# Performance work log

Hardware: AMD Instinct MI355X
Metric: run time of the kernel (lower is better)

## Reference

```python
import jax, jax.numpy as jnp
import numpy as np

N1, E1 = 102400, 300000
N2, E2 = 10240, 40960
N3, E3 = 1024, 4096
G = 64
D = 256   # node_dim == hidden_dim (forced by where(M==0, x, M))
B = 64    # bond_dim
DEPTHS = (3, 3, 4)


def _make_edges(rng, n_nodes, n_edges):
    # build mirrored directed edges so every edge has an exact reverse
    half = n_edges // 2
    u = rng.integers(0, n_nodes, half)
    v = rng.integers(0, n_nodes, half)
    src = np.concatenate([u, v])
    dst = np.concatenate([v, u])
    rev = np.concatenate([np.arange(half, n_edges), np.arange(0, half)])
    return np.stack([src, dst]).astype(np.int64), rev.astype(np.int64)


def _linear_params(key, fan_in, fan_out):
    k1, k2 = jax.random.split(key)
    s = 1.0 / np.sqrt(fan_in)
    W = jax.random.uniform(k1, (fan_in, fan_out), jnp.float32, -s, s)
    b = jax.random.uniform(k2, (fan_out,), jnp.float32, -s, s)
    return W, b


def setup_inputs() -> dict:
    rng = np.random.default_rng(0)
    key = jax.random.key(0)
    ks = jax.random.split(key, 16)

    ei1, rev1 = _make_edges(rng, N1, E1)
    ei2, rev2 = _make_edges(rng, N2, E2)
    ei3, rev3 = _make_edges(rng, N3, E3)

    inp = {
        "x": jax.random.normal(ks[0], (N1, D), jnp.float32),
        "edge_attr1": jax.random.normal(ks[1], (E1, B), jnp.float32),
        "edge_attr2": jax.random.normal(ks[2], (E2, B), jnp.float32),
        "edge_attr3": jax.random.normal(ks[3], (E3, B), jnp.float32),
        "edge_index1": jnp.asarray(ei1), "rev_edge_index1": jnp.asarray(rev1),
        "edge_index2": jnp.asarray(ei2), "rev_edge_index2": jnp.asarray(rev2),
        "edge_index3": jnp.asarray(ei3), "rev_edge_index3": jnp.asarray(rev3),
        "batch1_2": jnp.asarray(np.repeat(np.arange(N2), N1 // N2)),
        "batch2": jnp.asarray(np.repeat(np.arange(N3), N2 // N3)),
        "batch3": jnp.asarray(np.repeat(np.arange(G), N3 // G)),
    }
    kidx = 4
    for lvl in (1, 2, 3):
        Wi, bi = _linear_params(ks[kidx], D + B, D); kidx += 1
        Wh, bh = _linear_params(ks[kidx], D, D); kidx += 1
        Wo, bo = _linear_params(ks[kidx], D + D, D); kidx += 1
        inp[f"Wi{lvl}"], inp[f"bi{lvl}"] = Wi, bi
        inp[f"Wh{lvl}"], inp[f"bh{lvl}"] = Wh, bh
        inp[f"Wo{lvl}"], inp[f"bo{lvl}"] = Wo, bo
    return inp


def _bmp(x, src, dst, rev, ea, Wi, bi, Wh, bh, Wo, bo, depth):
    # BondMessagePassing.forward (dropout is identity in eval)
    n = x.shape[0]
    H0 = jax.nn.relu(jnp.concatenate([x[src], ea], axis=1) @ Wi + bi)  # [E, D]
    H = H0
    for _ in range(depth - 1):
        agg = jax.ops.segment_sum(H, dst, num_segments=n)              # [N, D]
        M = agg[src] - H[rev]
        H = jax.nn.relu(H0 + M @ Wh + bh)
    M = jax.ops.segment_sum(H, dst, num_segments=n)
    M = jnp.where(jnp.sum(M, axis=1, keepdims=True) == 0, x, M)
    return jax.nn.relu(jnp.concatenate([x, M], axis=1) @ Wo + bo)


def _mean_pool(h, seg, n):
    s = jax.ops.segment_sum(h, seg, num_segments=n)
    c = jax.ops.segment_sum(jnp.ones((h.shape[0], 1), h.dtype), seg, num_segments=n)
    return s / jnp.maximum(c, 1.0)


def reference(x, edge_attr1, edge_attr2, edge_attr3,
              edge_index1, rev_edge_index1, edge_index2, rev_edge_index2,
              edge_index3, rev_edge_index3, batch1_2, batch2, batch3,
              Wi1, bi1, Wh1, bh1, Wo1, bo1,
              Wi2, bi2, Wh2, bh2, Wo2, bo2,
              Wi3, bi3, Wh3, bh3, Wo3, bo3):
    h1 = _bmp(x, edge_index1[0], edge_index1[1], rev_edge_index1, edge_attr1,
              Wi1, bi1, Wh1, bh1, Wo1, bo1, DEPTHS[0])
    x2 = _mean_pool(h1, batch1_2, N2)
    h2 = _bmp(x2, edge_index2[0], edge_index2[1], rev_edge_index2, edge_attr2,
              Wi2, bi2, Wh2, bh2, Wo2, bo2, DEPTHS[1])
    x3 = _mean_pool(h2, batch2, N3)
    h3 = _bmp(x3, edge_index3[0], edge_index3[1], rev_edge_index3, edge_attr3,
              Wi3, bi3, Wh3, bh3, Wo3, bo3, DEPTHS[2])
    out = _mean_pool(h3, batch3, G)  # [G, D] subgraph3_pooled
    return out
```

## Files before the change

### kernel.cpp

```cpp
#include <hip/hip_runtime.h>
#include <stdint.h>

typedef __bf16 bf16;
typedef __bf16 bf16x4 __attribute__((ext_vector_type(4)));
typedef __bf16 bf16x8 __attribute__((ext_vector_type(8)));
typedef float  f32x4  __attribute__((ext_vector_type(4)));

__device__ __forceinline__ int clampi(int v, int n) { return (v < 0 || v >= n) ? 0 : v; }

__global__ void wtcvt_kernel(const float* __restrict__ W, bf16* __restrict__ Wt, int K) {
  int idx = blockIdx.x * 256 + threadIdx.x;
  if (idx >= K * 256) return;
  int k = idx >> 8, n = idx & 255;
  Wt[(size_t)n * K + k] = (bf16)W[idx];
}

__global__ void hist_kernel(const int* __restrict__ dst, int E, int* __restrict__ cnt, int N) {
  int e = blockIdx.x * 256 + threadIdx.x;
  if (e < E) atomicAdd(&cnt[clampi(dst[e], N)], 1);
}

__global__ void scan_block_kernel(const int* __restrict__ cnt, int N,
                                  int* __restrict__ incl, int* __restrict__ bsums) {
  __shared__ int sd[256];
  int t = threadIdx.x, bid = blockIdx.x;
  int base = bid * 1024 + t * 4;
  int v0 = (base + 0 < N) ? cnt[base + 0] : 0;
  int v1 = (base + 1 < N) ? cnt[base + 1] : 0;
  int v2 = (base + 2 < N) ? cnt[base + 2] : 0;
  int v3 = (base + 3 < N) ? cnt[base + 3] : 0;
  int s1 = v0 + v1, s2 = s1 + v2, s3 = s2 + v3;
  sd[t] = s3;
  __syncthreads();
  for (int off = 1; off < 256; off <<= 1) {
    int x = 0;
    if (t >= off) x = sd[t - off];
    __syncthreads();
    sd[t] += x;
    __syncthreads();
  }
  int excl = sd[t] - s3;
  if (base + 0 < N) incl[base + 0] = excl + v0;
  if (base + 1 < N) incl[base + 1] = excl + s1;
  if (base + 2 < N) incl[base + 2] = excl + s2;
  if (base + 3 < N) incl[base + 3] = excl + s3;
  if (t == 255) bsums[bid] = sd[255];
}

__global__ void scan_sums_kernel(const int* __restrict__ bsums, int nb, int* __restrict__ bexcl) {
  __shared__ int sd[256];
  int t = threadIdx.x;
  int v = (t < nb) ? bsums[t] : 0;
  sd[t] = v;
  __syncthreads();
  for (int off = 1; off < 256; off <<= 1) {
    int x = 0;
    if (t >= off) x = sd[t - off];
    __syncthreads();
    sd[t] += x;
    __syncthreads();
  }
  if (t < nb) bexcl[t] = sd[t] - v;
}

__global__ void scan_add_kernel(const int* __restrict__ incl, const int* __restrict__ bexcl,
                                int N, int* __restrict__ offs) {
  int i = blockIdx.x * 256 + threadIdx.x;
  if (i < N) offs[i + 1] = incl[i] + bexcl[i >> 10];
  if (i == 0) offs[0] = 0;
}

__global__ void scatter_kernel(const int* __restrict__ dst, int E, const int* __restrict__ offs,
                               int* __restrict__ cursor, int* __restrict__ elist, int N) {
  int e = blockIdx.x * 256 + threadIdx.x;
  if (e < E) {
    int d = clampi(dst[e], N);
    int p = atomicAdd(&cursor[d], 1);
    elist[offs[d] + p] = e;
  }
}

template <int WHERE, int XF32>
__global__ void segsum_kernel(const bf16* __restrict__ H, const int* __restrict__ elist,
                              const int* __restrict__ offs, const float* __restrict__ xf,
                              const bf16* __restrict__ xb, bf16* __restrict__ out, int N) {
  int lane = threadIdx.x & 63;
  int node = blockIdx.x * 4 + (threadIdx.x >> 6);
  if (node >= N) return;
  int beg = offs[node], end = offs[node + 1];
  float a0 = 0.f, a1 = 0.f, a2 = 0.f, a3 = 0.f;
  for (int p = beg; p < end; ++p) {
    int e = elist[p];
    bf16x4 v = ((const bf16x4*)(H + (size_t)e * 256))[lane];
    a0 += (float)v[0]; a1 += (float)v[1]; a2 += (float)v[2]; a3 += (float)v[3];
  }
  if (WHERE) {
    float s = a0 + a1 + a2 + a3;
    for (int off = 1; off < 64; off <<= 1) s += __shfl_xor(s, off);
    if (s == 0.f) {
      bf16x4 o;
      if (XF32) {
        float4 xv = ((const float4*)(xf))[(size_t)node * 64 + lane];
        o[0] = (bf16)xv.x; o[1] = (bf16)xv.y; o[2] = (bf16)xv.z; o[3] = (bf16)xv.w;
      } else {
        o = ((const bf16x4*)(xb + (size_t)node * 256))[lane];
      }
      ((bf16x4*)(out + (size_t)node * 256))[lane] = o;
      return;
    }
  }
  bf16x4 o = {(bf16)a0, (bf16)a1, (bf16)a2, (bf16)a3};
  ((bf16x4*)(out + (size_t)node * 256))[lane] = o;
}

template <int OUTF32>
__global__ void pool_kernel(const bf16* __restrict__ h, bf16* __restrict__ outb,
                            float* __restrict__ outf, int Nout, int cnt) {
  int lane = threadIdx.x & 63;
  int node = blockIdx.x * 4 + (threadIdx.x >> 6);
  if (node >= Nout) return;
  float a0 = 0.f, a1 = 0.f, a2 = 0.f, a3 = 0.f;
  size_t base = (size_t)node * cnt;
  for (int p = 0; p < cnt; ++p) {
    bf16x4 v = ((const bf16x4*)(h + (base + p) * 256))[lane];
    a0 += (float)v[0]; a1 += (float)v[1]; a2 += (float)v[2]; a3 += (float)v[3];
  }
  float c = (float)cnt;
  a0 /= c; a1 /= c; a2 /= c; a3 /= c;
  if (OUTF32) {
    float4 o = {a0, a1, a2, a3};
    ((float4*)(outf + (size_t)node * 256))[lane] = o;
  } else {
    bf16x4 o = {(bf16)a0, (bf16)a1, (bf16)a2, (bf16)a3};
    ((bf16x4*)(outb + (size_t)node * 256))[lane] = o;
  }
}

template <int MODE, int XF32>
__global__ __launch_bounds__(256, 2) void gemm_kernel(
    const float* __restrict__ A1f, const bf16* __restrict__ A1b,
    const float* __restrict__ A2f, const bf16* __restrict__ A2b,
    const bf16* __restrict__ Wt, const float* __restrict__ bias, const bf16* H0,
    const int* __restrict__ srcIdx, const int* __restrict__ revIdx,
    bf16* out, int Mrows, int K, int Nsrc) {
  __shared__ __align__(16) bf16 As[128 * 64];
  __shared__ __align__(16) bf16 Bs[128 * 64];
  int tid = threadIdx.x;
  int lane = tid & 63;
  int wave = tid >> 6;
  int wm = wave >> 1, wn = wave & 1;
  int m0 = blockIdx.x * 128;
  int n0 = blockIdx.y * 128;

  f32x4 acc[4][4];
#pragma unroll
  for (int i = 0; i < 4; ++i)
#pragma unroll
    for (int j = 0; j < 4; ++j) acc[i][j] = (f32x4){0.f, 0.f, 0.f, 0.f};

  int nk = K / 64;
  for (int kc = 0; kc < nk; ++kc) {
    int k0 = kc * 64;
    __syncthreads();
#pragma unroll
    for (int r = 0; r < 4; ++r) {
      int unit = r * 256 + tid;
      int row = unit >> 3, u = unit & 7, us = u ^ (row & 7);
      bf16x8 v = *(const bf16x8*)(Wt + (size_t)(n0 + row) * K + k0 + u * 8);
      *(bf16x8*)(&Bs[(size_t)(row * 8 + us) * 8]) = v;
    }
#pragma unroll
    for (int r = 0; r < 4; ++r) {
      int unit = r * 256 + tid;
      int row = unit >> 3, u = unit & 7, us = u ^ (row & 7);
      int rr = m0 + row;
      if (rr >= Mrows) rr = Mrows - 1;
      bf16x8 v;
      if (MODE == 0) {
        if (k0 < 256) {
          int sn = clampi(srcIdx[rr], Nsrc);
          if (XF32) {
            const float* g = A1f + (size_t)sn * 256 + k0 + u * 8;
            float4 a = *(const float4*)g, b = *(const float4*)(g + 4);
            v[0] = (bf16)a.x; v[1] = (bf16)a.y; v[2] = (bf16)a.z; v[3] = (bf16)a.w;
            v[4] = (bf16)b.x; v[5] = (bf16)b.y; v[6] = (bf16)b.z; v[7] = (bf16)b.w;
          } else {
            v = *(const bf16x8*)(A1b + (size_t)sn * 256 + k0 + u * 8);
          }
        } else {
          const float* g = A2f + (size_t)rr * 64 + (k0 - 256) + u * 8;
          float4 a = *(const float4*)g, b = *(const float4*)(g + 4);
          v[0] = (bf16)a.x; v[1] = (bf16)a.y; v[2] = (bf16)a.z; v[3] = (bf16)a.w;
          v[4] = (bf16)b.x; v[5] = (bf16)b.y; v[6] = (bf16)b.z; v[7] = (bf16)b.w;
        }
      } else if (MODE == 1) {
        int sn = clampi(srcIdx[rr], Nsrc);
        int rv = clampi(revIdx[rr], Mrows);
        bf16x8 va = *(const bf16x8*)(A1b + (size_t)sn * 256 + k0 + u * 8);
        bf16x8 vh = *(const bf16x8*)(A2b + (size_t)rv * 256 + k0 + u * 8);
#pragma unroll
        for (int j = 0; j < 8; ++j) v[j] = (bf16)((float)va[j] - (float)vh[j]);
      } else {
        if (k0 < 256) {
          if (XF32) {
            const float* g = A1f + (size_t)rr * 256 + k0 + u * 8;
            float4 a = *(const float4*)g, b = *(const float4*)(g + 4);
            v[0] = (bf16)a.x; v[1] = (bf16)a.y; v[2] = (bf16)a.z; v[3] = (bf16)a.w;
            v[4] = (bf16)b.x; v[5] = (bf16)b.y; v[6] = (bf16)b.z; v[7] = (bf16)b.w;
          } else {
            v = *(const bf16x8*)(A1b + (size_t)rr * 256 + k0 + u * 8);
          }
        } else {
          v = *(const bf16x8*)(A2b + (size_t)rr * 256 + (k0 - 256) + u * 8);
        }
      }
      *(bf16x8*)(&As[(size_t)(row * 8 + us) * 8]) = v;
    }
    __syncthreads();
#pragma unroll
    for (int s = 0; s < 2; ++s) {
      int kq = s * 4 + (lane >> 4);
      bf16x8 af[4], bfr[4];
#pragma unroll
      for (int i = 0; i < 4; ++i) {
        int arow = wm * 64 + i * 16 + (lane & 15);
        af[i] = *(const bf16x8*)(&As[(size_t)arow * 64 + (size_t)(kq ^ (arow & 7)) * 8]);
      }
#pragma unroll
      for (int j = 0; j < 4; ++j) {
        int brow = wn * 64 + j * 16 + (lane & 15);
        bfr[j] = *(const bf16x8*)(&Bs[(size_t)brow * 64 + (size_t)(kq ^ (brow & 7)) * 8]);
      }
#pragma unroll
      for (int i = 0; i < 4; ++i)
#pragma unroll
        for (int j = 0; j < 4; ++j)
          acc[i][j] = __builtin_amdgcn_mfma_f32_16x16x32_bf16(af[i], bfr[j], acc[i][j], 0, 0, 0);
    }
  }
#pragma unroll
  for (int i = 0; i < 4; ++i) {
    int rbase = m0 + wm * 64 + i * 16 + ((lane >> 4) << 2);
#pragma unroll
    for (int j = 0; j < 4; ++j) {
      int col = n0 + wn * 64 + j * 16 + (lane & 15);
      float bcol = bias[col];
#pragma unroll
      for (int r = 0; r < 4; ++r) {
        int row = rbase + r;
        if (row < Mrows) {
          float v = acc[i][j][r] + bcol;
          if (MODE == 1) v += (float)H0[(size_t)row * 256 + col];
          v = fmaxf(v, 0.f);
          out[(size_t)row * 256 + col] = (bf16)v;
        }
      }
    }
  }
}

template <int XF32>
static void run_level(const float* xf, const bf16* xb, const float* ea,
                      const int* src, const int* dst, const int* rev, int E, int N, int depth,
                      const bf16* WiT, const float* bi_, const bf16* WhT, const float* bh_,
                      const bf16* WoT, const float* bo_,
                      bf16* C, bf16* Dd, bf16* Ee, bf16* agg, bf16* h,
                      int* cnt, int* incl, int* offs, int* cursr, int* bsums, int* bexcl,
                      int* elist, hipStream_t stream) {
  hipMemsetAsync(cnt, 0, (size_t)N * 4, stream);
  hist_kernel<<<(E + 255) / 256, 256, 0, stream>>>(dst, E, cnt, N);
  int nb = (N + 1023) / 1024;
  scan_block_kernel<<<nb, 256, 0, stream>>>(cnt, N, incl, bsums);
  scan_sums_kernel<<<1, 256, 0, stream>>>(bsums, nb, bexcl);
  scan_add_kernel<<<(N + 255) / 256, 256, 0, stream>>>(incl, bexcl, N, offs);
  hipMemsetAsync(cursr, 0, (size_t)N * 4, stream);
  scatter_kernel<<<(E + 255) / 256, 256, 0, stream>>>(dst, E, offs, cursr, elist, N);

  dim3 ge((E + 127) / 128, 2);
  gemm_kernel<0, XF32><<<ge, 256, 0, stream>>>(xf, xb, ea, nullptr, WiT, bi_, nullptr, src,
                                               nullptr, C, E, 320, N);
  bf16* Hcur = C;
  for (int it = 0; it < depth - 1; ++it) {
    segsum_kernel<0, 0><<<(N + 3) / 4, 256, 0, stream>>>(Hcur, elist, offs, nullptr, nullptr,
                                                         agg, N);
    bf16* Hn = (it == depth - 2) ? C : ((it & 1) ? Ee : Dd);
    gemm_kernel<1, 0><<<ge, 256, 0, stream>>>(nullptr, agg, nullptr, Hcur, WhT, bh_, C, src,
                                              rev, Hn, E, 256, N);
    Hcur = Hn;
  }
  segsum_kernel<1, XF32><<<(N + 3) / 4, 256, 0, stream>>>(Hcur, elist, offs, xf, xb, agg, N);
  dim3 gn((N + 127) / 128, 2);
  gemm_kernel<2, XF32><<<gn, 256, 0, stream>>>(xf, xb, nullptr, agg, WoT, bo_, nullptr, nullptr,
                                               nullptr, h, N, 512, N);
}

extern "C" void kernel_launch(void* const* d_in, const int* in_sizes, int n_in,
                              void* d_out, int out_size, void* d_ws, size_t ws_size,
                              hipStream_t stream) {
  constexpr int N1 = 102400, E1 = 300000;
  constexpr int N2 = 10240, E2 = 40960;
  constexpr int N3 = 1024, E3 = 4096;
  constexpr int G = 64;
  constexpr int KI = 320, KH = 256, KO = 512;

  const float* x   = (const float*)d_in[0];
  const float* ea1 = (const float*)d_in[1];
  const float* ea2 = (const float*)d_in[2];
  const float* ea3 = (const float*)d_in[3];
  const int* ei1 = (const int*)d_in[4];
  const int* rv1 = (const int*)d_in[5];
  const int* ei2 = (const int*)d_in[6];
  const int* rv2 = (const int*)d_in[7];
  const int* ei3 = (const int*)d_in[8];
  const int* rv3 = (const int*)d_in[9];
  const float *Wi[3], *bi[3], *Wh[3], *bh[3], *Wo[3], *bo[3];
  for (int l = 0; l < 3; ++l) {
    Wi[l] = (const float*)d_in[13 + 6 * l + 0];
    bi[l] = (const float*)d_in[13 + 6 * l + 1];
    Wh[l] = (const float*)d_in[13 + 6 * l + 2];
    bh[l] = (const float*)d_in[13 + 6 * l + 3];
    Wo[l] = (const float*)d_in[13 + 6 * l + 4];
    bo[l] = (const float*)d_in[13 + 6 * l + 5];
  }
  float* outp = (float*)d_out;
  char* ws = (char*)d_ws;

  size_t off = 0;
  auto alloc = [&](size_t b) { size_t o = off; off += (b + 255) & ~(size_t)255; return o; };
  size_t o_wit[3], o_wht[3], o_wot[3];
  for (int l = 0; l < 3; ++l) {
    o_wit[l] = alloc((size_t)256 * KI * 2);
    o_wht[l] = alloc((size_t)256 * KH * 2);
    o_wot[l] = alloc((size_t)256 * KO * 2);
  }
  size_t o_C   = alloc((size_t)E1 * 256 * 2);
  size_t o_D   = alloc((size_t)E1 * 256 * 2);
  size_t o_E3b = alloc((size_t)E3 * 256 * 2);
  size_t o_agg = alloc((size_t)N1 * 256 * 2);
  size_t o_x2  = alloc((size_t)N2 * 256 * 2);
  size_t o_h2  = alloc((size_t)N2 * 256 * 2);
  size_t o_x3  = alloc((size_t)N3 * 256 * 2);
  size_t o_h3  = alloc((size_t)N3 * 256 * 2);
  size_t o_cnt = alloc((size_t)N1 * 4);
  size_t o_inc = alloc((size_t)N1 * 4);
  size_t o_off = alloc((size_t)(N1 + 1) * 4);
  size_t o_cur = alloc((size_t)N1 * 4);
  size_t o_bs  = alloc(1024 * 4);
  size_t o_bx  = alloc(1024 * 4);
  size_t o_el  = alloc((size_t)E1 * 4);

  if (ws_size < off) {
    hipMemsetAsync(d_out, 0, (size_t)out_size * 4, stream);
    return;
  }

  int* cnt   = (int*)(ws + o_cnt);
  int* incl  = (int*)(ws + o_inc);
  int* offs  = (int*)(ws + o_off);
  int* cursr = (int*)(ws + o_cur);
  int* bsums = (int*)(ws + o_bs);
  int* bexcl = (int*)(ws + o_bx);
  int* elist = (int*)(ws + o_el);
  bf16* C    = (bf16*)(ws + o_C);
  bf16* Dd   = (bf16*)(ws + o_D);
  bf16* E3b  = (bf16*)(ws + o_E3b);
  bf16* agg  = (bf16*)(ws + o_agg);
  bf16* x2b  = (bf16*)(ws + o_x2);
  bf16* h2b  = (bf16*)(ws + o_h2);
  bf16* x3b  = (bf16*)(ws + o_x3);
  bf16* h3b  = (bf16*)(ws + o_h3);

  for (int l = 0; l < 3; ++l) {
    wtcvt_kernel<<<(KI * 256 + 255) / 256, 256, 0, stream>>>(Wi[l], (bf16*)(ws + o_wit[l]), KI);
    wtcvt_kernel<<<(KH * 256 + 255) / 256, 256, 0, stream>>>(Wh[l], (bf16*)(ws + o_wht[l]), KH);
    wtcvt_kernel<<<(KO * 256 + 255) / 256, 256, 0, stream>>>(Wo[l], (bf16*)(ws + o_wot[l]), KO);
  }

  run_level<1>(x, nullptr, ea1, ei1, ei1 + E1, rv1, E1, N1, 3,
               (bf16*)(ws + o_wit[0]), bi[0], (bf16*)(ws + o_wht[0]), bh[0],
               (bf16*)(ws + o_wot[0]), bo[0], C, Dd, Dd, agg, C,
               cnt, incl, offs, cursr, bsums, bexcl, elist, stream);
  pool_kernel<0><<<(N2 + 3) / 4, 256, 0, stream>>>(C, x2b, nullptr, N2, N1 / N2);

  run_level<0>(nullptr, x2b, ea2, ei2, ei2 + E2, rv2, E2, N2, 3,
               (bf16*)(ws + o_wit[1]), bi[1], (bf16*)(ws + o_wht[1]), bh[1],
               (bf16*)(ws + o_wot[1]), bo[1], C, Dd, Dd, agg, h2b,
               cnt, incl, offs, cursr, bsums, bexcl, elist, stream);
  pool_kernel<0><<<(N3 + 3) / 4, 256, 0, stream>>>(h2b, x3b, nullptr, N3, N2 / N3);

  run_level<0>(nullptr, x3b, ea3, ei3, ei3 + E3, rv3, E3, N3, 4,
               (bf16*)(ws + o_wit[2]), bi[2], (bf16*)(ws + o_wht[2]), bh[2],
               (bf16*)(ws + o_wot[2]), bo[2], C, Dd, E3b, agg, h3b,
               cnt, incl, offs, cursr, bsums, bexcl, elist, stream);
  pool_kernel<1><<<(G + 3) / 4, 256, 0, stream>>>(h3b, nullptr, outp, G, N3 / G);
}
```

Before: 1.436 ms.

## Widen GEMM tile to full output width with async B loads and A prefetch

The GEMM now uses 512-thread blocks covering all 256 output columns, so each gathered A row is fetched once instead of twice across two column blocks. B tiles are loaded directly into LDS with global_load_lds, and the next K-chunk's A data is prefetched into registers while MFMAs run on the current chunk. Gather indices are computed once per block. The costs are more LDS per block (As plus a doubled Bs), more register pressure from the prefetch buffers, and a harder occupancy target of 4 blocks of 512 threads.

```diff
diff --git a/kernel.cpp b/kernel.cpp
--- a/kernel.cpp
+++ b/kernel.cpp
@@ -7,6 +7,11 @@
 typedef float  f32x4  __attribute__((ext_vector_type(4)));
 
 __device__ __forceinline__ int clampi(int v, int n) { return (v < 0 || v >= n) ? 0 : v; }
+
+__device__ __forceinline__ void gload16(const void* g, void* l) {
+  __builtin_amdgcn_global_load_lds((const __attribute__((address_space(1))) void*)g,
+                                   (__attribute__((address_space(3))) void*)l, 16, 0, 0);
+}
 
 __global__ void wtcvt_kernel(const float* __restrict__ W, bf16* __restrict__ Wt, int K) {
   int idx = blockIdx.x * 256 + threadIdx.x;
@@ -137,20 +142,40 @@
 }
 
 template <int MODE, int XF32>
-__global__ __launch_bounds__(256, 2) void gemm_kernel(
+__global__ __launch_bounds__(512, 4) void gemm_kernel(
     const float* __restrict__ A1f, const bf16* __restrict__ A1b,
     const float* __restrict__ A2f, const bf16* __restrict__ A2b,
     const bf16* __restrict__ Wt, const float* __restrict__ bias, const bf16* H0,
     const int* __restrict__ srcIdx, const int* __restrict__ revIdx,
     bf16* out, int Mrows, int K, int Nsrc) {
   __shared__ __align__(16) bf16 As[128 * 64];
-  __shared__ __align__(16) bf16 Bs[128 * 64];
+  __shared__ __align__(16) bf16 Bs[256 * 64];
   int tid = threadIdx.x;
   int lane = tid & 63;
   int wave = tid >> 6;
-  int wm = wave >> 1, wn = wave & 1;
+  int wm = wave >> 2, wn = wave & 3;
   int m0 = blockIdx.x * 128;
-  int n0 = blockIdx.y * 128;
+
+  int rowA[2], uA[2];
+  int base1[2], base2[2];
+#pragma unroll
+  for (int r = 0; r < 2; ++r) {
+    int unit = r * 512 + tid;
+    rowA[r] = unit >> 3;
+    uA[r] = unit & 7;
+    int rr = m0 + rowA[r];
+    if (rr >= Mrows) rr = Mrows - 1;
+    if (MODE == 0) {
+      base1[r] = clampi(srcIdx[rr], Nsrc) * 256;
+      base2[r] = rr * 64;
+    } else if (MODE == 1) {
+      base1[r] = clampi(srcIdx[rr], Nsrc) * 256;
+      base2[r] = clampi(revIdx[rr], Mrows) * 256;
+    } else {
+      base1[r] = rr * 256;
+      base2[r] = rr * 256;
+    }
+  }
 
   f32x4 acc[4][4];
 #pragma unroll
@@ -158,65 +183,92 @@
 #pragma unroll
     for (int j = 0; j < 4; ++j) acc[i][j] = (f32x4){0.f, 0.f, 0.f, 0.f};
 
-  int nk = K / 64;
-  for (int kc = 0; kc < nk; ++kc) {
+  float4 pf[2][2];
+
+  auto loadA = [&](int kc) {
     int k0 = kc * 64;
-    __syncthreads();
-#pragma unroll
-    for (int r = 0; r < 4; ++r) {
-      int unit = r * 256 + tid;
-      int row = unit >> 3, u = unit & 7, us = u ^ (row & 7);
-      bf16x8 v = *(const bf16x8*)(Wt + (size_t)(n0 + row) * K + k0 + u * 8);
-      *(bf16x8*)(&Bs[(size_t)(row * 8 + us) * 8]) = v;
-    }
-#pragma unroll
-    for (int r = 0; r < 4; ++r) {
-      int unit = r * 256 + tid;
-      int row = unit >> 3, u = unit & 7, us = u ^ (row & 7);
-      int rr = m0 + row;
-      if (rr >= Mrows) rr = Mrows - 1;
-      bf16x8 v;
+#pragma unroll
+    for (int r = 0; r < 2; ++r) {
+      int u8 = uA[r] * 8;
       if (MODE == 0) {
         if (k0 < 256) {
-          int sn = clampi(srcIdx[rr], Nsrc);
           if (XF32) {
-            const float* g = A1f + (size_t)sn * 256 + k0 + u * 8;
-            float4 a = *(const float4*)g, b = *(const float4*)(g + 4);
-            v[0] = (bf16)a.x; v[1] = (bf16)a.y; v[2] = (bf16)a.z; v[3] = (bf16)a.w;
-            v[4] = (bf16)b.x; v[5] = (bf16)b.y; v[6] = (bf16)b.z; v[7] = (bf16)b.w;
+            const float* g = A1f + (size_t)(base1[r] + k0 + u8);
+            pf[r][0] = *(const float4*)g;
+            pf[r][1] = *(const float4*)(g + 4);
           } else {
-            v = *(const bf16x8*)(A1b + (size_t)sn * 256 + k0 + u * 8);
+            pf[r][0] = *(const float4*)(A1b + (size_t)(base1[r] + k0 + u8));
           }
         } else {
-          const float* g = A2f + (size_t)rr * 64 + (k0 - 256) + u * 8;
-          float4 a = *(const float4*)g, b = *(const float4*)(g + 4);
-          v[0] = (bf16)a.x; v[1] = (bf16)a.y; v[2] = (bf16)a.z; v[3] = (bf16)a.w;
-          v[4] = (bf16)b.x; v[5] = (bf16)b.y; v[6] = (bf16)b.z; v[7] = (bf16)b.w;
+          const float* g = A2f + (size_t)(base2[r] + u8);
+          pf[r][0] = *(const float4*)g;
+          pf[r][1] = *(const float4*)(g + 4);
         }
       } else if (MODE == 1) {
-        int sn = clampi(srcIdx[rr], Nsrc);
-        int rv = clampi(revIdx[rr], Mrows);
-        bf16x8 va = *(const bf16x8*)(A1b + (size_t)sn * 256 + k0 + u * 8);
-        bf16x8 vh = *(const bf16x8*)(A2b + (size_t)rv * 256 + k0 + u * 8);
-#pragma unroll
-        for (int j = 0; j < 8; ++j) v[j] = (bf16)((float)va[j] - (float)vh[j]);
+        pf[r][0] = *(const float4*)(A1b + (size_t)(base1[r] + k0 + u8));
+        pf[r][1] = *(const float4*)(A2b + (size_t)(base2[r] + k0 + u8));
       } else {
         if (k0 < 256) {
           if (XF32) {
-            const float* g = A1f + (size_t)rr * 256 + k0 + u * 8;
-            float4 a = *(const float4*)g, b = *(const float4*)(g + 4);
-            v[0] = (bf16)a.x; v[1] = (bf16)a.y; v[2] = (bf16)a.z; v[3] = (bf16)a.w;
-            v[4] = (bf16)b.x; v[5] = (bf16)b.y; v[6] = (bf16)b.z; v[7] = (bf16)b.w;
+            const float* g = A1f + (size_t)(base1[r] + k0 + u8);
+            pf[r][0] = *(const float4*)g;
+            pf[r][1] = *(const float4*)(g + 4);
           } else {
-            v = *(const bf16x8*)(A1b + (size_t)rr * 256 + k0 + u * 8);
+            pf[r][0] = *(const float4*)(A1b + (size_t)(base1[r] + k0 + u8));
           }
         } else {
-          v = *(const bf16x8*)(A2b + (size_t)rr * 256 + (k0 - 256) + u * 8);
+          pf[r][0] = *(const float4*)(A2b + (size_t)(base2[r] + (k0 - 256) + u8));
         }
       }
+    }
+  };
+
+  auto writeA = [&](int kc) {
+    int k0 = kc * 64;
+#pragma unroll
+    for (int r = 0; r < 2; ++r) {
+      int row = rowA[r], us = uA[r] ^ (row & 7);
+      bf16x8 v;
+      bool cvt32;
+      if (MODE == 0) cvt32 = XF32 || (k0 >= 256);
+      else if (MODE == 2) cvt32 = XF32 && (k0 < 256);
+      else cvt32 = false;
+      if (MODE == 1) {
+        bf16x8 va = *(bf16x8*)(&pf[r][0]);
+        bf16x8 vh = *(bf16x8*)(&pf[r][1]);
+#pragma unroll
+        for (int j = 0; j < 8; ++j) v[j] = (bf16)((float)va[j] - (float)vh[j]);
+      } else if (cvt32) {
+        const float* f = (const float*)&pf[r][0];
+#pragma unroll
+        for (int j = 0; j < 8; ++j) v[j] = (bf16)f[j];
+      } else {
+        v = *(bf16x8*)(&pf[r][0]);
+      }
       *(bf16x8*)(&As[(size_t)(row * 8 + us) * 8]) = v;
     }
-    __syncthreads();
+  };
+
+  auto loadB = [&](int kc) {
+    int k0 = kc * 64;
+#pragma unroll
+    for (int r = 0; r < 4; ++r) {
+      int unit = r * 512 + tid;
+      int row = unit >> 3, us = (unit & 7) ^ (row & 7);
+      const bf16* g = Wt + (size_t)row * K + k0 + us * 8;
+      bf16* l = &Bs[(size_t)(r * 512 + wave * 64) * 8];
+      gload16(g, l);
+    }
+  };
+
+  int nk = K / 64;
+  loadA(0);
+  for (int kc = 0; kc < nk; ++kc) {
+    __syncthreads();
+    writeA(kc);
+    loadB(kc);
+    __syncthreads();
+    if (kc + 1 < nk) loadA(kc + 1);
 #pragma unroll
     for (int s = 0; s < 2; ++s) {
       int kq = s * 4 + (lane >> 4);
@@ -243,7 +295,7 @@
     int rbase = m0 + wm * 64 + i * 16 + ((lane >> 4) << 2);
 #pragma unroll
     for (int j = 0; j < 4; ++j) {
-      int col = n0 + wn * 64 + j * 16 + (lane & 15);
+      int col = wn * 64 + j * 16 + (lane & 15);
       float bcol = bias[col];
 #pragma unroll
       for (int r = 0; r < 4; ++r) {
@@ -276,21 +328,21 @@
   hipMemsetAsync(cursr, 0, (size_t)N * 4, stream);
   scatter_kernel<<<(E + 255) / 256, 256, 0, stream>>>(dst, E, offs, cursr, elist, N);
 
-  dim3 ge((E + 127) / 128, 2);
-  gemm_kernel<0, XF32><<<ge, 256, 0, stream>>>(xf, xb, ea, nullptr, WiT, bi_, nullptr, src,
+  dim3 ge((E + 127) / 128);
+  gemm_kernel<0, XF32><<<ge, 512, 0, stream>>>(xf, xb, ea, nullptr, WiT, bi_, nullptr, src,
                                                nullptr, C, E, 320, N);
   bf16* Hcur = C;
   for (int it = 0; it < depth - 1; ++it) {
     segsum_kernel<0, 0><<<(N + 3) / 4, 256, 0, stream>>>(Hcur, elist, offs, nullptr, nullptr,
                                                          agg, N);
     bf16* Hn = (it == depth - 2) ? C : ((it & 1) ? Ee : Dd);
-    gemm_kernel<1, 0><<<ge, 256, 0, stream>>>(nullptr, agg, nullptr, Hcur, WhT, bh_, C, src,
+    gemm_kernel<1, 0><<<ge, 512, 0, stream>>>(nullptr, agg, nullptr, Hcur, WhT, bh_, C, src,
                                               rev, Hn, E, 256, N);
     Hcur = Hn;
   }
   segsum_kernel<1, XF32><<<(N + 3) / 4, 256, 0, stream>>>(Hcur, elist, offs, xf, xb, agg, N);
-  dim3 gn((N + 127) / 128, 2);
-  gemm_kernel<2, XF32><<<gn, 256, 0, stream>>>(xf, xb, nullptr, agg, WoT, bo_, nullptr, nullptr,
+  dim3 gn((N + 127) / 128);
+  gemm_kernel<2, XF32><<<gn, 512, 0, stream>>>(xf, xb, nullptr, agg, WoT, bo_, nullptr, nullptr,
                                                nullptr, h, N, 512, N);
 }
 
```

Result: faster. 1.290 ms (-10.2%).

## Restructure GEMMs to load full-K A tile once and split concatenated weights

Applied to the files above, without the earlier changes.

Replaces the single templated GEMM, which used a 2D grid over column halves and a K loop, with a full-row kernel. Each block now loads its whole 128x256 A tile (the gathered, or gathered-minus-reverse, rows) into LDS once and reuses it for both 128-column halves of the output, so the irregular gather is no longer repeated per column block. Weight tiles are fetched with direct global-to-LDS loads. The concatenated-input GEMMs are split into two passes, an edge-attribute GEMM and an x GEMM, with the first result added in the second pass's epilogue. This adds an extra round trip of a bf16 intermediate through global memory and uses about 128KB of LDS per block, which limits occupancy.

```diff
diff --git a/kernel.cpp b/kernel.cpp
--- a/kernel.cpp
+++ b/kernel.cpp
@@ -8,11 +8,17 @@
 
 __device__ __forceinline__ int clampi(int v, int n) { return (v < 0 || v >= n) ? 0 : v; }
 
-__global__ void wtcvt_kernel(const float* __restrict__ W, bf16* __restrict__ Wt, int K) {
+__device__ __forceinline__ void gload16(const void* g, void* l) {
+  __builtin_amdgcn_global_load_lds((const __attribute__((address_space(1))) void*)g,
+                                   (__attribute__((address_space(3))) void*)l, 16, 0, 0);
+}
+
+__global__ void wtcvtT_kernel(const float* __restrict__ W, bf16* __restrict__ Wt,
+                              int krows, int krow0) {
   int idx = blockIdx.x * 256 + threadIdx.x;
-  if (idx >= K * 256) return;
+  if (idx >= krows * 256) return;
   int k = idx >> 8, n = idx & 255;
-  Wt[(size_t)n * K + k] = (bf16)W[idx];
+  Wt[(size_t)n * krows + k] = (bf16)W[(size_t)(krow0 + k) * 256 + n];
 }
 
 __global__ void hist_kernel(const int* __restrict__ dst, int E, int* __restrict__ cnt, int N) {
@@ -136,134 +142,217 @@
   }
 }
 
-template <int MODE, int XF32>
-__global__ __launch_bounds__(256, 2) void gemm_kernel(
-    const float* __restrict__ A1f, const bf16* __restrict__ A1b,
-    const float* __restrict__ A2f, const bf16* __restrict__ A2b,
-    const bf16* __restrict__ Wt, const float* __restrict__ bias, const bf16* H0,
-    const int* __restrict__ srcIdx, const int* __restrict__ revIdx,
-    bf16* out, int Mrows, int K, int Nsrc) {
+__global__ __launch_bounds__(512) void gemm_ea(
+    const float* __restrict__ ea, const bf16* __restrict__ Wt ,
+    const float* __restrict__ bias, bf16* __restrict__ out, int Mrows) {
   __shared__ __align__(16) bf16 As[128 * 64];
-  __shared__ __align__(16) bf16 Bs[128 * 64];
-  int tid = threadIdx.x;
-  int lane = tid & 63;
-  int wave = tid >> 6;
-  int wm = wave >> 1, wn = wave & 1;
-  int m0 = blockIdx.x * 128;
-  int n0 = blockIdx.y * 128;
-
+  __shared__ __align__(16) bf16 Bs[256 * 64];
+  const int tid = threadIdx.x;
+  const int lane = tid & 63;
+  const int wave = tid >> 6;
+  const int wm = wave >> 2, wn = wave & 3;
+  const int m0 = blockIdx.x * 128;
+
+#pragma unroll
+  for (int r = 0; r < 2; ++r) {
+    int unit = r * 512 + tid;
+    int row = unit >> 3, u = unit & 7;
+    int rr = m0 + row;
+    if (rr >= Mrows) rr = Mrows - 1;
+    const float* g = ea + (size_t)rr * 64 + u * 8;
+    float4 a = *(const float4*)g, b = *(const float4*)(g + 4);
+    bf16x8 v = {(bf16)a.x, (bf16)a.y, (bf16)a.z, (bf16)a.w,
+                (bf16)b.x, (bf16)b.y, (bf16)b.z, (bf16)b.w};
+    int pos = u ^ (row & 7);
+    *(bf16x8*)(&As[((size_t)row * 8 + pos) * 8]) = v;
+  }
+#pragma unroll
+  for (int r = 0; r < 4; ++r) {
+    int unit = r * 512 + tid;
+    int col = unit >> 3, u = unit & 7;
+    int us = u ^ (col & 7);
+    gload16(Wt + (size_t)col * 64 + us * 8, &Bs[(size_t)(r * 512 + wave * 64) * 8]);
+  }
   f32x4 acc[4][4];
 #pragma unroll
   for (int i = 0; i < 4; ++i)
 #pragma unroll
     for (int j = 0; j < 4; ++j) acc[i][j] = (f32x4){0.f, 0.f, 0.f, 0.f};
-
-  int nk = K / 64;
-  for (int kc = 0; kc < nk; ++kc) {
-    int k0 = kc * 64;
-    __syncthreads();
-#pragma unroll
-    for (int r = 0; r < 4; ++r) {
-      int unit = r * 256 + tid;
-      int row = unit >> 3, u = unit & 7, us = u ^ (row & 7);
-      bf16x8 v = *(const bf16x8*)(Wt + (size_t)(n0 + row) * K + k0 + u * 8);
-      *(bf16x8*)(&Bs[(size_t)(row * 8 + us) * 8]) = v;
-    }
-#pragma unroll
-    for (int r = 0; r < 4; ++r) {
-      int unit = r * 256 + tid;
-      int row = unit >> 3, u = unit & 7, us = u ^ (row & 7);
-      int rr = m0 + row;
-      if (rr >= Mrows) rr = Mrows - 1;
-      bf16x8 v;
-      if (MODE == 0) {
-        if (k0 < 256) {
-          int sn = clampi(srcIdx[rr], Nsrc);
-          if (XF32) {
-            const float* g = A1f + (size_t)sn * 256 + k0 + u * 8;
-            float4 a = *(const float4*)g, b = *(const float4*)(g + 4);
-            v[0] = (bf16)a.x; v[1] = (bf16)a.y; v[2] = (bf16)a.z; v[3] = (bf16)a.w;
-            v[4] = (bf16)b.x; v[5] = (bf16)b.y; v[6] = (bf16)b.z; v[7] = (bf16)b.w;
-          } else {
-            v = *(const bf16x8*)(A1b + (size_t)sn * 256 + k0 + u * 8);
-          }
-        } else {
-          const float* g = A2f + (size_t)rr * 64 + (k0 - 256) + u * 8;
-          float4 a = *(const float4*)g, b = *(const float4*)(g + 4);
-          v[0] = (bf16)a.x; v[1] = (bf16)a.y; v[2] = (bf16)a.z; v[3] = (bf16)a.w;
-          v[4] = (bf16)b.x; v[5] = (bf16)b.y; v[6] = (bf16)b.z; v[7] = (bf16)b.w;
-        }
-      } else if (MODE == 1) {
-        int sn = clampi(srcIdx[rr], Nsrc);
-        int rv = clampi(revIdx[rr], Mrows);
-        bf16x8 va = *(const bf16x8*)(A1b + (size_t)sn * 256 + k0 + u * 8);
-        bf16x8 vh = *(const bf16x8*)(A2b + (size_t)rv * 256 + k0 + u * 8);
-#pragma unroll
-        for (int j = 0; j < 8; ++j) v[j] = (bf16)((float)va[j] - (float)vh[j]);
-      } else {
-        if (k0 < 256) {
-          if (XF32) {
-            const float* g = A1f + (size_t)rr * 256 + k0 + u * 8;
-            float4 a = *(const float4*)g, b = *(const float4*)(g + 4);
-            v[0] = (bf16)a.x; v[1] = (bf16)a.y; v[2] = (bf16)a.z; v[3] = (bf16)a.w;
-            v[4] = (bf16)b.x; v[5] = (bf16)b.y; v[6] = (bf16)b.z; v[7] = (bf16)b.w;
-          } else {
-            v = *(const bf16x8*)(A1b + (size_t)rr * 256 + k0 + u * 8);
-          }
-        } else {
-          v = *(const bf16x8*)(A2b + (size_t)rr * 256 + (k0 - 256) + u * 8);
-        }
-      }
-      *(bf16x8*)(&As[(size_t)(row * 8 + us) * 8]) = v;
-    }
-    __syncthreads();
-#pragma unroll
-    for (int s = 0; s < 2; ++s) {
-      int kq = s * 4 + (lane >> 4);
-      bf16x8 af[4], bfr[4];
-#pragma unroll
-      for (int i = 0; i < 4; ++i) {
-        int arow = wm * 64 + i * 16 + (lane & 15);
-        af[i] = *(const bf16x8*)(&As[(size_t)arow * 64 + (size_t)(kq ^ (arow & 7)) * 8]);
-      }
-#pragma unroll
-      for (int j = 0; j < 4; ++j) {
-        int brow = wn * 64 + j * 16 + (lane & 15);
-        bfr[j] = *(const bf16x8*)(&Bs[(size_t)brow * 64 + (size_t)(kq ^ (brow & 7)) * 8]);
-      }
-#pragma unroll
-      for (int i = 0; i < 4; ++i)
-#pragma unroll
-        for (int j = 0; j < 4; ++j)
-          acc[i][j] = __builtin_amdgcn_mfma_f32_16x16x32_bf16(af[i], bfr[j], acc[i][j], 0, 0, 0);
-    }
+  __syncthreads();
+#pragma unroll
+  for (int s = 0; s < 2; ++s) {
+    int kq = s * 4 + (lane >> 4);
+    bf16x8 af[4], bfr[4];
+#pragma unroll
+    for (int i = 0; i < 4; ++i) {
+      int ar = wm * 64 + i * 16 + (lane & 15);
+      af[i] = *(const bf16x8*)(&As[((size_t)ar * 8 + (kq ^ (ar & 7))) * 8]);
+    }
+#pragma unroll
+    for (int j = 0; j < 4; ++j) {
+      int bc = wn * 64 + j * 16 + (lane & 15);
+      bfr[j] = *(const bf16x8*)(&Bs[((size_t)bc * 8 + (kq ^ (bc & 7))) * 8]);
+    }
+#pragma unroll
+    for (int i = 0; i < 4; ++i)
+#pragma unroll
+      for (int j = 0; j < 4; ++j)
+        acc[i][j] = __builtin_amdgcn_mfma_f32_16x16x32_bf16(af[i], bfr[j], acc[i][j], 0, 0, 0);
   }
 #pragma unroll
   for (int i = 0; i < 4; ++i) {
     int rbase = m0 + wm * 64 + i * 16 + ((lane >> 4) << 2);
 #pragma unroll
     for (int j = 0; j < 4; ++j) {
-      int col = n0 + wn * 64 + j * 16 + (lane & 15);
+      int col = wn * 64 + j * 16 + (lane & 15);
       float bcol = bias[col];
 #pragma unroll
       for (int r = 0; r < 4; ++r) {
         int row = rbase + r;
-        if (row < Mrows) {
-          float v = acc[i][j][r] + bcol;
-          if (MODE == 1) v += (float)H0[(size_t)row * 256 + col];
-          v = fmaxf(v, 0.f);
-          out[(size_t)row * 256 + col] = (bf16)v;
+        if (row < Mrows) out[(size_t)row * 256 + col] = (bf16)(acc[i][j][r] + bcol);
+      }
+    }
+  }
+}
+
+template <int SRC, int XF32, int ADDROW, int RELU>
+__global__ __launch_bounds__(512) void gemm_fullB(
+    const float* __restrict__ Af, const bf16* __restrict__ Ab, const bf16* __restrict__ Hb,
+    const bf16* __restrict__ Wt , const float* __restrict__ bias,
+    const bf16* __restrict__ addrow, const int* __restrict__ srcIdx,
+    const int* __restrict__ revIdx, bf16* out, int Mrows, int Nsrc) {
+  __shared__ __align__(16) bf16 As[128 * 256];
+  __shared__ __align__(16) bf16 Bs[128 * 256];
+  const int tid = threadIdx.x;
+  const int lane = tid & 63;
+  const int wave = tid >> 6;
+  const int wm = wave >> 2, wn = wave & 3;
+  const int m0 = blockIdx.x * 128;
+
+  const int rid = tid >> 3, lane8 = tid & 7;
+#pragma unroll
+  for (int rp = 0; rp < 2; ++rp) {
+    int row = rp * 64 + rid;
+    int rr = m0 + row;
+    if (rr >= Mrows) rr = Mrows - 1;
+    int swz = lane8 ^ (row & 7);
+    if (SRC == 2) {
+      const bf16* ga = Ab + (size_t)clampi(srcIdx[rr], Nsrc) * 256;
+      const bf16* gh = Hb + (size_t)clampi(revIdx[rr], Mrows) * 256;
+      float4 pa[4], ph[4];
+#pragma unroll
+      for (int st = 0; st < 4; ++st) {
+        pa[st] = *(const float4*)(ga + (lane8 + 8 * st) * 8);
+        ph[st] = *(const float4*)(gh + (lane8 + 8 * st) * 8);
+      }
+#pragma unroll
+      for (int st = 0; st < 4; ++st) {
+        bf16x8 va = *(bf16x8*)&pa[st];
+        bf16x8 vh = *(bf16x8*)&ph[st];
+        bf16x8 v;
+#pragma unroll
+        for (int j = 0; j < 8; ++j) v[j] = (bf16)((float)va[j] - (float)vh[j]);
+        *(bf16x8*)(&As[((size_t)row * 32 + st * 8 + swz) * 8]) = v;
+      }
+    } else {
+      int rsrc = (SRC == 1) ? clampi(srcIdx[rr], Nsrc) : rr;
+      if (XF32) {
+        const float* g = Af + (size_t)rsrc * 256;
+        float4 p[4][2];
+#pragma unroll
+        for (int st = 0; st < 4; ++st) {
+          const float* gg = g + (lane8 + 8 * st) * 8;
+          p[st][0] = *(const float4*)gg;
+          p[st][1] = *(const float4*)(gg + 4);
         }
-      }
-    }
+#pragma unroll
+        for (int st = 0; st < 4; ++st) {
+          const float* f = (const float*)&p[st][0];
+          bf16x8 v;
+#pragma unroll
+          for (int j = 0; j < 8; ++j) v[j] = (bf16)f[j];
+          *(bf16x8*)(&As[((size_t)row * 32 + st * 8 + swz) * 8]) = v;
+        }
+      } else {
+        const bf16* g = Ab + (size_t)rsrc * 256;
+        float4 p[4];
+#pragma unroll
+        for (int st = 0; st < 4; ++st) p[st] = *(const float4*)(g + (lane8 + 8 * st) * 8);
+#pragma unroll
+        for (int st = 0; st < 4; ++st)
+          *(bf16x8*)(&As[((size_t)row * 32 + st * 8 + swz) * 8]) = *(bf16x8*)&p[st];
+      }
+    }
+  }
+
+  f32x4 acc[4][2];
+#pragma unroll
+  for (int p = 0; p < 2; ++p) {
+#pragma unroll
+    for (int r = 0; r < 8; ++r) {
+      int unit = r * 512 + tid;
+      int col = unit >> 5, cu = unit & 31;
+      int cus = (cu & 24) | ((cu & 7) ^ (col & 7));
+      gload16(Wt + (size_t)(p * 128 + col) * 256 + cus * 8,
+              &Bs[(size_t)(r * 512 + wave * 64) * 8]);
+    }
+#pragma unroll
+    for (int i = 0; i < 4; ++i)
+#pragma unroll
+      for (int j = 0; j < 2; ++j) acc[i][j] = (f32x4){0.f, 0.f, 0.f, 0.f};
+    __syncthreads();
+#pragma unroll
+    for (int kc = 0; kc < 4; ++kc) {
+#pragma unroll
+      for (int s = 0; s < 2; ++s) {
+        int kq = s * 4 + (lane >> 4);
+        bf16x8 af[4], bfr[2];
+#pragma unroll
+        for (int i = 0; i < 4; ++i) {
+          int ar = wm * 64 + i * 16 + (lane & 15);
+          af[i] = *(const bf16x8*)(&As[((size_t)ar * 32 + kc * 8 + (kq ^ (ar & 7))) * 8]);
+        }
+#pragma unroll
+        for (int j = 0; j < 2; ++j) {
+          int bc = wn * 32 + j * 16 + (lane & 15);
+          bfr[j] = *(const bf16x8*)(&Bs[((size_t)bc * 32 + kc * 8 + (kq ^ (bc & 7))) * 8]);
+        }
+#pragma unroll
+        for (int i = 0; i < 4; ++i)
+#pragma unroll
+          for (int j = 0; j < 2; ++j)
+            acc[i][j] = __builtin_amdgcn_mfma_f32_16x16x32_bf16(af[i], bfr[j], acc[i][j], 0, 0, 0);
+      }
+    }
+#pragma unroll
+    for (int i = 0; i < 4; ++i) {
+      int rbase = m0 + wm * 64 + i * 16 + ((lane >> 4) << 2);
+#pragma unroll
+      for (int j = 0; j < 2; ++j) {
+        int col = p * 128 + wn * 32 + j * 16 + (lane & 15);
+        float bcol = bias ? bias[col] : 0.f;
+#pragma unroll
+        for (int r = 0; r < 4; ++r) {
+          int row = rbase + r;
+          if (row < Mrows) {
+            float v = acc[i][j][r] + bcol;
+            if (ADDROW) v += (float)addrow[(size_t)row * 256 + col];
+            if (RELU) v = fmaxf(v, 0.f);
+            out[(size_t)row * 256 + col] = (bf16)v;
+          }
+        }
+      }
+    }
+    if (p == 0) __syncthreads();
   }
 }
 
 template <int XF32>
 static void run_level(const float* xf, const bf16* xb, const float* ea,
                       const int* src, const int* dst, const int* rev, int E, int N, int depth,
-                      const bf16* WiT, const float* bi_, const bf16* WhT, const float* bh_,
-                      const bf16* WoT, const float* bo_,
+                      const bf16* WixT, const bf16* WieT, const float* bi_,
+                      const bf16* WhT, const float* bh_,
+                      const bf16* WoxT, const bf16* WomT, const float* bo_,
                       bf16* C, bf16* Dd, bf16* Ee, bf16* agg, bf16* h,
                       int* cnt, int* incl, int* offs, int* cursr, int* bsums, int* bexcl,
                       int* elist, hipStream_t stream) {
@@ -276,22 +365,25 @@
   hipMemsetAsync(cursr, 0, (size_t)N * 4, stream);
   scatter_kernel<<<(E + 255) / 256, 256, 0, stream>>>(dst, E, offs, cursr, elist, N);
 
-  dim3 ge((E + 127) / 128, 2);
-  gemm_kernel<0, XF32><<<ge, 256, 0, stream>>>(xf, xb, ea, nullptr, WiT, bi_, nullptr, src,
-                                               nullptr, C, E, 320, N);
+  dim3 ge((E + 127) / 128);
+  gemm_ea<<<ge, 512, 0, stream>>>(ea, WieT, bi_, Dd, E);
+  gemm_fullB<1, XF32, 1, 1><<<ge, 512, 0, stream>>>(xf, xb, nullptr, WixT, nullptr, Dd, src,
+                                                    nullptr, C, E, N);
   bf16* Hcur = C;
   for (int it = 0; it < depth - 1; ++it) {
     segsum_kernel<0, 0><<<(N + 3) / 4, 256, 0, stream>>>(Hcur, elist, offs, nullptr, nullptr,
                                                          agg, N);
     bf16* Hn = (it == depth - 2) ? C : ((it & 1) ? Ee : Dd);
-    gemm_kernel<1, 0><<<ge, 256, 0, stream>>>(nullptr, agg, nullptr, Hcur, WhT, bh_, C, src,
-                                              rev, Hn, E, 256, N);
+    gemm_fullB<2, 0, 1, 1><<<ge, 512, 0, stream>>>(nullptr, agg, Hcur, WhT, bh_, C, src, rev,
+                                                   Hn, E, N);
     Hcur = Hn;
   }
   segsum_kernel<1, XF32><<<(N + 3) / 4, 256, 0, stream>>>(Hcur, elist, offs, xf, xb, agg, N);
-  dim3 gn((N + 127) / 128, 2);
-  gemm_kernel<2, XF32><<<gn, 256, 0, stream>>>(xf, xb, nullptr, agg, WoT, bo_, nullptr, nullptr,
-                                               nullptr, h, N, 512, N);
+  dim3 gn((N + 127) / 128);
+  gemm_fullB<0, XF32, 0, 0><<<gn, 512, 0, stream>>>(xf, xb, nullptr, WoxT, bo_, nullptr,
+                                                    nullptr, nullptr, Dd, N, N);
+  gemm_fullB<0, 0, 1, 1><<<gn, 512, 0, stream>>>(nullptr, agg, nullptr, WomT, nullptr, Dd,
+                                                 nullptr, nullptr, h, N, N);
 }
 
 extern "C" void kernel_launch(void* const* d_in, const int* in_sizes, int n_in,
@@ -301,7 +393,6 @@
   constexpr int N2 = 10240, E2 = 40960;
   constexpr int N3 = 1024, E3 = 4096;
   constexpr int G = 64;
-  constexpr int KI = 320, KH = 256, KO = 512;
 
   const float* x   = (const float*)d_in[0];
   const float* ea1 = (const float*)d_in[1];
@@ -327,11 +418,13 @@
 
   size_t off = 0;
   auto alloc = [&](size_t b) { size_t o = off; off += (b + 255) & ~(size_t)255; return o; };
-  size_t o_wit[3], o_wht[3], o_wot[3];
+  size_t o_wix[3], o_wie[3], o_wh[3], o_wox[3], o_wom[3];
   for (int l = 0; l < 3; ++l) {
-    o_wit[l] = alloc((size_t)256 * KI * 2);
-    o_wht[l] = alloc((size_t)256 * KH * 2);
-    o_wot[l] = alloc((size_t)256 * KO * 2);
+    o_wix[l] = alloc((size_t)256 * 256 * 2);
+    o_wie[l] = alloc((size_t)256 * 64 * 2);
+    o_wh[l]  = alloc((size_t)256 * 256 * 2);
+    o_wox[l] = alloc((size_t)256 * 256 * 2);
+    o_wom[l] = alloc((size_t)256 * 256 * 2);
   }
   size_t o_C   = alloc((size_t)E1 * 256 * 2);
   size_t o_D   = alloc((size_t)E1 * 256 * 2);
@@ -371,26 +464,39 @@
   bf16* h3b  = (bf16*)(ws + o_h3);
 
   for (int l = 0; l < 3; ++l) {
-    wtcvt_kernel<<<(KI * 256 + 255) / 256, 256, 0, stream>>>(Wi[l], (bf16*)(ws + o_wit[l]), KI);
-    wtcvt_kernel<<<(KH * 256 + 255) / 256, 256, 0, stream>>>(Wh[l], (bf16*)(ws + o_wht[l]), KH);
-    wtcvt_kernel<<<(KO * 256 + 255) / 256, 256, 0, stream>>>(Wo[l], (bf16*)(ws + o_wot[l]), KO);
+    wtcvtT_kernel<<<(256 * 256 + 255) / 256, 256, 0, stream>>>(Wi[l], (bf16*)(ws + o_wix[l]),
+                                                               256, 0);
+    wtcvtT_kernel<<<(64 * 256 + 255) / 256, 256, 0, stream>>>(Wi[l], (bf16*)(ws + o_wie[l]),
+                                                              64, 256);
+    wtcvtT_kernel<<<(256 * 256 + 255) / 256, 256, 0, stream>>>(Wh[l], (bf16*)(ws + o_wh[l]),
+                                                               256, 0);
+    wtcvtT_kernel<<<(256 * 256 + 255) / 256, 256, 0, stream>>>(Wo[l], (bf16*)(ws + o_wox[l]),
+                                                               256, 0);
+    wtcvtT_kernel<<<(256 * 256 + 255) / 256, 256, 0, stream>>>(Wo[l], (bf16*)(ws + o_wom[l]),
+                                                               256, 256);
   }
 
   run_level<1>(x, nullptr, ea1, ei1, ei1 + E1, rv1, E1, N1, 3,
-               (bf16*)(ws + o_wit[0]), bi[0], (bf16*)(ws + o_wht[0]), bh[0],
-               (bf16*)(ws + o_wot[0]), bo[0], C, Dd, Dd, agg, C,
+               (bf16*)(ws + o_wix[0]), (bf16*)(ws + o_wie[0]), bi[0],
+               (bf16*)(ws + o_wh[0]), bh[0],
+               (bf16*)(ws + o_wox[0]), (bf16*)(ws + o_wom[0]), bo[0],
+               C, Dd, Dd, agg, C,
                cnt, incl, offs, cursr, bsums, bexcl, elist, stream);
   pool_kernel<0><<<(N2 + 3) / 4, 256, 0, stream>>>(C, x2b, nullptr, N2, N1 / N2);
 
   run_level<0>(nullptr, x2b, ea2, ei2, ei2 + E2, rv2, E2, N2, 3,
-               (bf16*)(ws + o_wit[1]), bi[1], (bf16*)(ws + o_wht[1]), bh[1],
-               (bf16*)(ws + o_wot[1]), bo[1], C, Dd, Dd, agg, h2b,
+               (bf16*)(ws + o_wix[1]), (bf16*)(ws + o_wie[1]), bi[1],
+               (bf16*)(ws + o_wh[1]), bh[1],
+               (bf16*)(ws + o_wox[1]), (bf16*)(ws + o_wom[1]), bo[1],
+               C, Dd, Dd, agg, h2b,
                cnt, incl, offs, cursr, bsums, bexcl, elist, stream);
   pool_kernel<0><<<(N3 + 3) / 4, 256, 0, stream>>>(h2b, x3b, nullptr, N3, N2 / N3);
 
   run_level<0>(nullptr, x3b, ea3, ei3, ei3 + E3, rv3, E3, N3, 4,
-               (bf16*)(ws + o_wit[2]), bi[2], (bf16*)(ws + o_wht[2]), bh[2],
-               (bf16*)(ws + o_wot[2]), bo[2], C, Dd, E3b, agg, h3b,
+               (bf16*)(ws + o_wix[2]), (bf16*)(ws + o_wie[2]), bi[2],
+               (bf16*)(ws + o_wh[2]), bh[2],
+               (bf16*)(ws + o_wox[2]), (bf16*)(ws + o_wom[2]), bo[2],
+               C, Dd, E3b, agg, h3b,
                cnt, incl, offs, cursr, bsums, bexcl, elist, stream);
   pool_kernel<1><<<(G + 3) / 4, 256, 0, stream>>>(h3b, nullptr, outp, G, N3 / G);
 }
```

After: 1.899 ms. 32.3% more time.
